# Optimization experiments

Hardware: AMD Instinct MI355X
Metric: run time of the kernel (lower is better)

## Reference

```python
import jax, jax.numpy as jnp
import numpy as np

N_NODES = 200000
N_HYPEREDGES = 50000
NNZ = 3200000
D = 128
LEAKY = 0.2


def setup_inputs() -> dict:
    key = jax.random.key(0)
    k1, k2, k3, k4 = jax.random.split(key, 4)
    embs = jax.random.normal(k1, (N_NODES, D), dtype=jnp.float32)
    vals = jax.random.uniform(k2, (NNZ,), dtype=jnp.float32)
    rows = jax.random.randint(k3, (NNZ,), 0, N_NODES, dtype=jnp.int32)
    cols = jax.random.randint(k4, (NNZ,), 0, N_HYPEREDGES, dtype=jnp.int32)
    return {
        "embs": embs,
        "vals": vals,
        "rows": rows,
        "cols": cols,
        "n_nodes": N_NODES,
        "n_hyperedges": N_HYPEREDGES,
    }


def reference(embs, vals, rows, cols, n_nodes, n_hyperedges):
    # adj is sparse COO: adj[rows[k], cols[k]] = vals[k], shape [n_nodes, n_hyperedges]
    # Step 1: he = adj.T @ embs  -> [n_hyperedges, D]
    he = jax.ops.segment_sum(embs[rows] * vals[:, None], cols,
                             num_segments=n_hyperedges)
    # Step 2: out = adj @ he     -> [n_nodes, D]
    out = jax.ops.segment_sum(he[cols] * vals[:, None], rows,
                              num_segments=n_nodes)
    # LeakyReLU(negative_slope=LEAKY)
    return jnp.where(out >= 0, out, LEAKY * out)
```

## Files before the change

### kernel.cpp

```cpp
#include <hip/hip_runtime.h>

#define DIM 128
#define LEAKY 0.2f
#define N_NODES_C 200000
#define N_HE_C 50000

#define NNZ_SLAB 8192
#define BIN_B 512
#define SEGC_PB 64
#define NB_C 782
#define SEGR_PB 256
#define NB_R 782
#define CAP_B 4608

typedef float f32x4 __attribute__((ext_vector_type(4)));

__device__ __forceinline__ unsigned bf16r(float f) {
    return (__float_as_uint(f) + 0x8000u) >> 16;
}
__device__ __forceinline__ float bf16lo(unsigned u) {
    return __uint_as_float((u & 0xFFFFu) << 16);
}
__device__ __forceinline__ float bf16hi(unsigned u) {
    return __uint_as_float(u & 0xFFFF0000u);
}

__global__ void convert_bf16(const f32x4* __restrict__ in, uint2* __restrict__ out, int n4) {
    int t = blockIdx.x * blockDim.x + threadIdx.x;
    if (t >= n4) return;
    f32x4 x = __builtin_nontemporal_load(in + t);
    out[t] = make_uint2((bf16r(x.y) << 16) | bf16r(x.x),
                        (bf16r(x.w) << 16) | bf16r(x.z));
}

__global__ void __launch_bounds__(BIN_B)
bin_append(const int* __restrict__ rows, const int* __restrict__ cols,
           const float* __restrict__ vals, int nnz,
           int* __restrict__ curC, int* __restrict__ curR,
           int2* __restrict__ stagC, int2* __restrict__ stagR) {
    __shared__ int cnt[NB_C + NB_R];
    for (int i = threadIdx.x; i < NB_C + NB_R; i += BIN_B) cnt[i] = 0;
    __syncthreads();
    int base = blockIdx.x * NNZ_SLAB;
    int end = base + NNZ_SLAB; if (end > nnz) end = nnz;
    for (int k = base + threadIdx.x; k < end; k += BIN_B) {
        atomicAdd(&cnt[cols[k] >> 6], 1);
        atomicAdd(&cnt[NB_C + (rows[k] >> 8)], 1);
    }
    __syncthreads();
    for (int i = threadIdx.x; i < NB_C; i += BIN_B) {
        int n = cnt[i];
        cnt[i] = n ? atomicAdd(&curC[i], n) : 0;
    }
    for (int i = threadIdx.x; i < NB_R; i += BIN_B) {
        int n = cnt[NB_C + i];
        cnt[NB_C + i] = n ? atomicAdd(&curR[i], n) : 0;
    }
    __syncthreads();
    for (int k = base + threadIdx.x; k < end; k += BIN_B) {
        int r = rows[k], c = cols[k];
        int v = __float_as_int(vals[k]);
        int bc = c >> 6;
        int oc = atomicAdd(&cnt[bc], 1);
        if (oc < CAP_B)
            stagC[(size_t)bc * CAP_B + oc] = make_int2(((c & 63) << 18) | r, v);
        int br = r >> 8;
        int orr = atomicAdd(&cnt[NB_C + br], 1);
        if (orr < CAP_B)
            stagR[(size_t)br * CAP_B + orr] = make_int2(((r & 255) << 16) | c, v);
    }
}

template <int SEG_PB, int LSHIFT, int MODE>
__global__ void __launch_bounds__(256)
bucket_sort(const int* __restrict__ cur, const int2* __restrict__ stag,
            unsigned* __restrict__ outPacked,
            int* __restrict__ startOut, int* __restrict__ endOut, int nseg) {
    __shared__ int2 ent[CAP_B];
    __shared__ int cnt[SEG_PB];
    __shared__ int scn[SEG_PB];
    int b = blockIdx.x;
    size_t lo = (size_t)b * CAP_B;
    int n = cur[b]; if (n > CAP_B) n = CAP_B;
    int t = threadIdx.x;
    for (int i = t; i < SEG_PB; i += 256) cnt[i] = 0;
    __syncthreads();
    for (int i = t; i < n; i += 256) {
        int2 e = stag[lo + i];
        ent[i] = e;
        atomicAdd(&cnt[e.x >> LSHIFT], 1);
    }
    __syncthreads();
    if (t < SEG_PB) scn[t] = cnt[t];
    __syncthreads();
    for (int off = 1; off < SEG_PB; off <<= 1) {
        int x = (t < SEG_PB) ? scn[t] : 0;
        int add = (t >= off && t < SEG_PB) ? scn[t - off] : 0;
        __syncthreads();
        if (t < SEG_PB) scn[t] = x + add;
        __syncthreads();
    }
    int segBase = b * SEG_PB;
    if (t < SEG_PB) {
        int excl = t ? scn[t - 1] : 0;
        if (segBase + t < nseg) {
            startOut[segBase + t] = (int)lo + excl;
            endOut[segBase + t]   = (int)lo + scn[t];
        }
        cnt[t] = excl;
    }
    __syncthreads();
    for (int i = t; i < n; i += 256) {
        int2 e = ent[i];
        int s = e.x >> LSHIFT;
        int pos = (int)lo + atomicAdd(&cnt[s], 1);
        unsigned w;
        if (MODE == 0) {
            unsigned v14 = ((unsigned)e.y + 0x10000u) >> 17;
            w = ((unsigned)(e.x & 0x3FFFF) << 14) | (v14 & 0x3FFFu);
        } else {
            unsigned vb = ((unsigned)e.y + 0x8000u) >> 16;
            w = ((unsigned)(e.x & 0xFFFF) << 16) | vb;
        }
        outPacked[pos] = w;
    }
}


__global__ void seg_pass1(const int* __restrict__ start, const int* __restrict__ end,
                          const unsigned* __restrict__ packed,
                          const unsigned* __restrict__ srcb, unsigned* __restrict__ dstb,
                          int nseg) {
    int wid = (int)((blockIdx.x * (unsigned)blockDim.x + threadIdx.x) >> 6);
    int lane = threadIdx.x & 63;
    if (wid >= nseg) return;
    int s = start[wid];
    int e = end[wid];
    float ax = 0.f, ay = 0.f;
    int j = s;
    for (; j + 8 <= e; j += 8) {
        #pragma unroll
        for (int u = 0; u < 8; ++u) {
            unsigned p = packed[j + u];
            unsigned w = srcb[(size_t)(p >> 14) * 64 + lane];
            float v = __uint_as_float((p & 0x3FFFu) << 17);
            ax += bf16lo(w) * v;
            ay += bf16hi(w) * v;
        }
    }
    for (; j < e; ++j) {
        unsigned p = packed[j];
        unsigned w = srcb[(size_t)(p >> 14) * 64 + lane];
        float v = __uint_as_float((p & 0x3FFFu) << 17);
        ax += bf16lo(w) * v;
        ay += bf16hi(w) * v;
    }
    dstb[(size_t)wid * 64 + lane] = (bf16r(ay) << 16) | bf16r(ax);
}

__global__ void seg_pass2(const int* __restrict__ start, const int* __restrict__ end,
                          const unsigned* __restrict__ packed,
                          const unsigned* __restrict__ srcb, float* __restrict__ dst,
                          int nseg) {
    int wid = (int)((blockIdx.x * (unsigned)blockDim.x + threadIdx.x) >> 6);
    int lane = threadIdx.x & 63;
    if (wid >= nseg) return;
    int s = start[wid];
    int e = end[wid];
    float ax = 0.f, ay = 0.f;
    int j = s;
    for (; j + 4 <= e; j += 4) {
        #pragma unroll
        for (int u = 0; u < 4; ++u) {
            unsigned p = packed[j + u];
            unsigned w = srcb[(size_t)(p >> 16) * 64 + lane];
            float v = __uint_as_float(p << 16);
            ax += bf16lo(w) * v;
            ay += bf16hi(w) * v;
        }
    }
    for (; j < e; ++j) {
        unsigned p = packed[j];
        unsigned w = srcb[(size_t)(p >> 16) * 64 + lane];
        float v = __uint_as_float(p << 16);
        ax += bf16lo(w) * v;
        ay += bf16hi(w) * v;
    }
    ax = ax >= 0.f ? ax : LEAKY * ax;
    ay = ay >= 0.f ? ay : LEAKY * ay;
    unsigned long long bits = ((unsigned long long)__float_as_uint(ay) << 32) |
                              (unsigned long long)__float_as_uint(ax);
    __builtin_nontemporal_store(bits,
        reinterpret_cast<unsigned long long*>(dst) + (size_t)wid * 64 + lane);
}

__global__ void scatter_step(const float* __restrict__ src, const float* __restrict__ vals,
                             const int* __restrict__ gidx, const int* __restrict__ sidx,
                             float* __restrict__ dst, int nnz) {
    long long t = (long long)blockIdx.x * blockDim.x + threadIdx.x;
    int k = (int)(t >> 5);
    if (k >= nnz) return;
    int q = ((int)t & 31) << 2;
    int g = gidx[k];
    int s = sidx[k];
    float v = vals[k];
    const float4 e = *reinterpret_cast<const float4*>(src + (size_t)g * DIM + q);
    float* dp = dst + (size_t)s * DIM + q;
    unsafeAtomicAdd(dp + 0, e.x * v);
    unsafeAtomicAdd(dp + 1, e.y * v);
    unsafeAtomicAdd(dp + 2, e.z * v);
    unsafeAtomicAdd(dp + 3, e.w * v);
}

__global__ void leaky_inplace(float* __restrict__ out, int n4) {
    int t = blockIdx.x * blockDim.x + threadIdx.x;
    if (t >= n4) return;
    float4* p = reinterpret_cast<float4*>(out) + t;
    float4 x = *p;
    x.x = x.x >= 0.f ? x.x : LEAKY * x.x;
    x.y = x.y >= 0.f ? x.y : LEAKY * x.y;
    x.z = x.z >= 0.f ? x.z : LEAKY * x.z;
    x.w = x.w >= 0.f ? x.w : LEAKY * x.w;
    *p = x;
}

extern "C" void kernel_launch(void* const* d_in, const int* in_sizes, int n_in,
                              void* d_out, int out_size, void* d_ws, size_t ws_size,
                              hipStream_t stream) {
    const float* embs = (const float*)d_in[0];
    const float* vals = (const float*)d_in[1];
    const int*   rows = (const int*)d_in[2];
    const int*   cols = (const int*)d_in[3];
    const int nnz = in_sizes[1];
    float* out = (float*)d_out;

    unsigned* embsB = (unsigned*)d_out;

    char* ws = (char*)d_ws;
    size_t off = 0;
    auto alloc = [&](size_t bytes) -> char* {
        char* p = ws + off;
        off = (off + bytes + 255) & ~(size_t)255;
        return p;
    };
    unsigned* heB   = (unsigned*)alloc((size_t)N_HE_C * DIM * 2);
    int* startC     = (int*)alloc((size_t)N_HE_C * sizeof(int));
    int* endC       = (int*)alloc((size_t)N_HE_C * sizeof(int));
    int* startR     = (int*)alloc((size_t)N_NODES_C * sizeof(int));
    int* endR       = (int*)alloc((size_t)N_NODES_C * sizeof(int));
    int* curC       = (int*)alloc((size_t)NB_C * sizeof(int));
    int* curR       = (int*)alloc((size_t)NB_R * sizeof(int));
    int2* stagC     = (int2*)alloc((size_t)NB_C * CAP_B * sizeof(int2));
    int2* stagR     = (int2*)alloc((size_t)NB_R * CAP_B * sizeof(int2));
    size_t required = off;

    if (ws_size < required) {
        float* he = (float*)d_ws;
        (void)hipMemsetAsync(he,  0, (size_t)N_HE_C * DIM * sizeof(float), stream);
        (void)hipMemsetAsync(out, 0, (size_t)N_NODES_C * DIM * sizeof(float), stream);
        long long nthreads = (long long)nnz * 32;
        dim3 grd((unsigned)((nthreads + 255) / 256));
        scatter_step<<<grd, 256, 0, stream>>>(embs, vals, rows, cols, he, nnz);
        scatter_step<<<grd, 256, 0, stream>>>(he, vals, cols, rows, out, nnz);
        int n4 = N_NODES_C * DIM / 4;
        leaky_inplace<<<(n4 + 255) / 256, 256, 0, stream>>>(out, n4);
        return;
    }

    (void)hipMemsetAsync(curC, 0, (size_t)NB_C * sizeof(int), stream);
    (void)hipMemsetAsync(curR, 0, (size_t)NB_R * sizeof(int), stream);

    int nslab = (nnz + NNZ_SLAB - 1) / NNZ_SLAB;
    bin_append<<<nslab, BIN_B, 0, stream>>>(rows, cols, vals, nnz,
                                            curC, curR, stagC, stagR);

    bucket_sort<SEGC_PB, 18, 0><<<NB_C, 256, 0, stream>>>(
        curC, stagC, (unsigned*)stagC, startC, endC, N_HE_C);
    bucket_sort<SEGR_PB, 16, 1><<<NB_R, 256, 0, stream>>>(
        curR, stagR, (unsigned*)stagR, startR, endR, N_NODES_C);

    {
        int n4 = N_NODES_C * DIM / 4;
        convert_bf16<<<(n4 + 255) / 256, 256, 0, stream>>>(
            (const f32x4*)embs, (uint2*)embsB, n4);
    }

    seg_pass1<<<(N_HE_C + 3) / 4, 256, 0, stream>>>(
        startC, endC, (const unsigned*)stagC, embsB, heB, N_HE_C);
    seg_pass2<<<(N_NODES_C + 3) / 4, 256, 0, stream>>>(
        startR, endR, (const unsigned*)stagR, heB, out, N_NODES_C);
}
```

Measured before the change: 409.8 us.

## Split binning per side and locally sort slabs in LDS for coalesced stores

Replaces the combined bin_append kernel with two per-side bin_side kernels, one for columns and one for rows. Each block sorts its slab of entries by bucket in shared memory, using a block-wide prefix scan over bucket counts, and only then writes them to the global staging buffers. Consecutive threads therefore store to contiguous runs within each bucket instead of scattered random addresses. The cost is reading rows/cols/vals twice across two launches, plus a larger shared-memory footprint that limits occupancy.

New measurement: 419.3 us. +2.3%, slower.

```diff
diff --git a/kernel.cpp b/kernel.cpp
--- a/kernel.cpp
+++ b/kernel.cpp
@@ -5,12 +5,10 @@
 #define N_NODES_C 200000
 #define N_HE_C 50000
 
-#define NNZ_SLAB 8192
-#define BIN_B 512
+#define SLAB2 11008
+#define NB 782
 #define SEGC_PB 64
-#define NB_C 782
 #define SEGR_PB 256
-#define NB_R 782
 #define CAP_B 4608
 
 typedef float f32x4 __attribute__((ext_vector_type(4)));
@@ -33,41 +31,68 @@
                         (bf16r(x.w) << 16) | bf16r(x.z));
 }
 
-__global__ void __launch_bounds__(BIN_B)
-bin_append(const int* __restrict__ rows, const int* __restrict__ cols,
-           const float* __restrict__ vals, int nnz,
-           int* __restrict__ curC, int* __restrict__ curR,
-           int2* __restrict__ stagC, int2* __restrict__ stagR) {
-    __shared__ int cnt[NB_C + NB_R];
-    for (int i = threadIdx.x; i < NB_C + NB_R; i += BIN_B) cnt[i] = 0;
-    __syncthreads();
-    int base = blockIdx.x * NNZ_SLAB;
-    int end = base + NNZ_SLAB; if (end > nnz) end = nnz;
-    for (int k = base + threadIdx.x; k < end; k += BIN_B) {
-        atomicAdd(&cnt[cols[k] >> 6], 1);
-        atomicAdd(&cnt[NB_C + (rows[k] >> 8)], 1);
-    }
-    __syncthreads();
-    for (int i = threadIdx.x; i < NB_C; i += BIN_B) {
-        int n = cnt[i];
-        cnt[i] = n ? atomicAdd(&curC[i], n) : 0;
-    }
-    for (int i = threadIdx.x; i < NB_R; i += BIN_B) {
-        int n = cnt[NB_C + i];
-        cnt[NB_C + i] = n ? atomicAdd(&curR[i], n) : 0;
-    }
-    __syncthreads();
-    for (int k = base + threadIdx.x; k < end; k += BIN_B) {
+template <int MODE>
+__global__ void __launch_bounds__(512)
+bin_side(const int* __restrict__ rows, const int* __restrict__ cols,
+         const float* __restrict__ vals, int nnz,
+         int* __restrict__ cur, int2* __restrict__ stag) {
+    __shared__ int2 sorted[SLAB2];
+    __shared__ unsigned short bkt[SLAB2];
+    __shared__ int cnt[NB];
+    __shared__ int scn[NB];
+    __shared__ int gb[NB];
+    __shared__ int part[512];
+    int t = threadIdx.x;
+    int base = blockIdx.x * SLAB2;
+    int nloc = nnz - base; if (nloc > SLAB2) nloc = SLAB2;
+    if (nloc < 0) nloc = 0;
+    for (int i = t; i < NB; i += 512) cnt[i] = 0;
+    __syncthreads();
+    for (int i = t; i < nloc; i += 512) {
+        int key = (MODE == 0) ? (cols[base + i] >> 6) : (rows[base + i] >> 8);
+        atomicAdd(&cnt[key], 1);
+    }
+    __syncthreads();
+    int c0 = (2 * t     < NB) ? cnt[2 * t]     : 0;
+    int c1 = (2 * t + 1 < NB) ? cnt[2 * t + 1] : 0;
+    part[t] = c0 + c1;
+    __syncthreads();
+    for (int off = 1; off < 512; off <<= 1) {
+        int x = part[t];
+        int add = (t >= off) ? part[t - off] : 0;
+        __syncthreads();
+        part[t] = x + add;
+        __syncthreads();
+    }
+    int pex = t ? part[t - 1] : 0;
+    if (2 * t < NB) {
+        scn[2 * t] = pex;
+        gb[2 * t] = c0 ? atomicAdd(&cur[2 * t], c0) : 0;
+    }
+    if (2 * t + 1 < NB) {
+        scn[2 * t + 1] = pex + c0;
+        gb[2 * t + 1] = c1 ? atomicAdd(&cur[2 * t + 1], c1) : 0;
+    }
+    __syncthreads();
+    for (int i = t; i < NB; i += 512) cnt[i] = scn[i];
+    __syncthreads();
+    for (int i = t; i < nloc; i += 512) {
+        int k = base + i;
         int r = rows[k], c = cols[k];
         int v = __float_as_int(vals[k]);
-        int bc = c >> 6;
-        int oc = atomicAdd(&cnt[bc], 1);
-        if (oc < CAP_B)
-            stagC[(size_t)bc * CAP_B + oc] = make_int2(((c & 63) << 18) | r, v);
-        int br = r >> 8;
-        int orr = atomicAdd(&cnt[NB_C + br], 1);
-        if (orr < CAP_B)
-            stagR[(size_t)br * CAP_B + orr] = make_int2(((r & 255) << 16) | c, v);
+        int key, x;
+        if (MODE == 0) { key = c >> 6; x = ((c & 63) << 18) | r; }
+        else           { key = r >> 8; x = ((r & 255) << 16) | c; }
+        int p = atomicAdd(&cnt[key], 1);
+        sorted[p] = make_int2(x, v);
+        bkt[p] = (unsigned short)key;
+    }
+    __syncthreads();
+    for (int i = t; i < nloc; i += 512) {
+        int b = bkt[i];
+        int off = gb[b] + (i - scn[b]);
+        if (off < CAP_B)
+            stag[(size_t)b * CAP_B + off] = sorted[i];
     }
 }
 
@@ -248,10 +273,10 @@
     int* endC       = (int*)alloc((size_t)N_HE_C * sizeof(int));
     int* startR     = (int*)alloc((size_t)N_NODES_C * sizeof(int));
     int* endR       = (int*)alloc((size_t)N_NODES_C * sizeof(int));
-    int* curC       = (int*)alloc((size_t)NB_C * sizeof(int));
-    int* curR       = (int*)alloc((size_t)NB_R * sizeof(int));
-    int2* stagC     = (int2*)alloc((size_t)NB_C * CAP_B * sizeof(int2));
-    int2* stagR     = (int2*)alloc((size_t)NB_R * CAP_B * sizeof(int2));
+    int* curC       = (int*)alloc((size_t)NB * sizeof(int));
+    int* curR       = (int*)alloc((size_t)NB * sizeof(int));
+    int2* stagC     = (int2*)alloc((size_t)NB * CAP_B * sizeof(int2));
+    int2* stagR     = (int2*)alloc((size_t)NB * CAP_B * sizeof(int2));
     size_t required = off;
 
     if (ws_size < required) {
@@ -267,16 +292,16 @@
         return;
     }
 
-    (void)hipMemsetAsync(curC, 0, (size_t)NB_C * sizeof(int), stream);
-    (void)hipMemsetAsync(curR, 0, (size_t)NB_R * sizeof(int), stream);
-
-    int nslab = (nnz + NNZ_SLAB - 1) / NNZ_SLAB;
-    bin_append<<<nslab, BIN_B, 0, stream>>>(rows, cols, vals, nnz,
-                                            curC, curR, stagC, stagR);
-
-    bucket_sort<SEGC_PB, 18, 0><<<NB_C, 256, 0, stream>>>(
+    (void)hipMemsetAsync(curC, 0, (size_t)NB * sizeof(int), stream);
+    (void)hipMemsetAsync(curR, 0, (size_t)NB * sizeof(int), stream);
+
+    int nslab = (nnz + SLAB2 - 1) / SLAB2;
+    bin_side<0><<<nslab, 512, 0, stream>>>(rows, cols, vals, nnz, curC, stagC);
+    bin_side<1><<<nslab, 512, 0, stream>>>(rows, cols, vals, nnz, curR, stagR);
+
+    bucket_sort<SEGC_PB, 18, 0><<<NB, 256, 0, stream>>>(
         curC, stagC, (unsigned*)stagC, startC, endC, N_HE_C);
-    bucket_sort<SEGR_PB, 16, 1><<<NB_R, 256, 0, stream>>>(
+    bucket_sort<SEGR_PB, 16, 1><<<NB, 256, 0, stream>>>(
         curR, stagR, (unsigned*)stagR, startR, endR, N_NODES_C);
 
     {
```
